# Optimization experiments

Hardware: AMD Instinct MI355X
Metric: run time of the kernel (lower is better)

## Reference

```python
import jax, jax.numpy as jnp
import numpy as np

MODEL_DIM = 1024
HEADS = 16
HEAD_DIM = MODEL_DIM // HEADS
SEQ = 1024


def setup_inputs() -> dict:
    key0 = jax.random.key(0)
    ks = jax.random.split(key0, 10)
    D, H, d, S = MODEL_DIM, HEADS, HEAD_DIM, SEQ
    s = 1.0 / np.sqrt(D)
    return {
        "value": jax.random.normal(ks[0], (S, D), dtype=jnp.float32),
        "key": jax.random.normal(ks[1], (S, D), dtype=jnp.float32),
        "query": jax.random.normal(ks[2], (S, D), dtype=jnp.float32),
        # per-head projection weights, torch Linear layout (out=d, in=D), stacked over heads
        "Wq": jax.random.uniform(ks[3], (H, d, D), jnp.float32, -s, s),
        "Wk": jax.random.uniform(ks[4], (H, d, D), jnp.float32, -s, s),
        "Wv": jax.random.uniform(ks[5], (H, d, D), jnp.float32, -s, s),
        # u, v biases: torch.rand -> uniform [0,1)
        "u": jax.random.uniform(ks[6], (H, d), dtype=jnp.float32),
        "v": jax.random.uniform(ks[7], (H, d), dtype=jnp.float32),
        "Wo": jax.random.uniform(ks[8], (D, D), jnp.float32, -s, s),
        "bo": jax.random.uniform(ks[9], (D,), jnp.float32, -s, s),
    }


def _rel_pos_R(d, Sq, Sk):
    # pos[i, j] = i - j (Transformer-XL style relative offsets)
    pos = (jnp.arange(Sq)[:, None] - jnp.arange(Sk)[None, :]).astype(jnp.float32)
    inv_freq = 10000.0 ** (-2.0 * jnp.arange(d // 2, dtype=jnp.float32) / d)  # (d/2,)
    ang = pos[None, :, :] * inv_freq[:, None, None]  # (d/2, Sq, Sk)
    # interleave: R[2i] = sin(ang_i), R[2i+1] = cos(ang_i)
    R = jnp.stack([jnp.sin(ang), jnp.cos(ang)], axis=1).reshape(d, Sq, Sk)
    return R


def reference(value, key, query, Wq, Wk, Wv, u, v, Wo, bo):
    # defaults of original forward: scale=True, mask=False
    H, d, D = Wq.shape
    Sq, Sk = query.shape[0], key.shape[0]
    q = jnp.einsum("hdD,sD->hsd", Wq, query)   # (H, Sq, d)
    k = jnp.einsum("hdD,tD->htd", Wk, key)     # (H, Sk, d)
    vals = jnp.einsum("hdD,tD->htd", Wv, value)  # (H, Sk, d)

    R = _rel_pos_R(d, Sq, Sk)  # (d, Sq, Sk)

    cc = jnp.einsum("hsd,htd->hst", q, k)       # content-content
    cp = jnp.einsum("hsd,dst->hst", q, R)       # content-position
    uk = jnp.einsum("hd,htd->ht", u, k)[:, None, :]  # global content bias
    vr = jnp.einsum("hd,dst->hst", v, R)        # global position bias

    att = (cc + cp + uk + vr) * (d ** -0.5)
    att = jax.nn.softmax(att, axis=2)

    out = jnp.einsum("hst,htd->hsd", att, vals)  # (H, Sq, d)
    out = out.transpose(1, 0, 2).reshape(Sq, H * d)  # concat heads along feature dim
    return out @ Wo.T + bo
```

## Files before the change

kernel.cpp:

```cpp
#include <hip/hip_runtime.h>
#include <math.h>

#define SQ 1024
#define DIM 1024
#define NH 16
#define HDIM 64

typedef short bf16x8 __attribute__((ext_vector_type(8)));
typedef float f32x4 __attribute__((ext_vector_type(4)));

__device__ __forceinline__ unsigned short f2bf(float x) {
  unsigned int u = __builtin_bit_cast(unsigned int, x);
  u += 0x7FFFu + ((u >> 16) & 1u);
  return (unsigned short)(u >> 16);
}
__device__ __forceinline__ unsigned int pkbf(float a, float b) {
  return (unsigned)f2bf(a) | ((unsigned)f2bf(b) << 16);
}

__global__ __launch_bounds__(256) void prep_kernel(
    const float* __restrict__ query, const float* __restrict__ key_,
    const float* __restrict__ value, const float* __restrict__ Wq,
    const float* __restrict__ Wk, const float* __restrict__ Wv,
    const float* __restrict__ Wo, unsigned short* __restrict__ bfin,
    unsigned short* __restrict__ Rc)
{
  const int b = blockIdx.x;
  if (b < 3584) {
    int gid = b * 256 + threadIdx.x;
    int seg = gid >> 17;
    int off = (gid & 131071) * 8;
    const float* s = seg == 0 ? query : seg == 1 ? key_ : seg == 2 ? value :
                     seg == 3 ? Wq : seg == 4 ? Wk : seg == 5 ? Wv : Wo;
    float4 a = *(const float4*)&s[off];
    float4 c = *(const float4*)&s[off + 4];
    uint4 o;
    o.x = pkbf(a.x, a.y); o.y = pkbf(a.z, a.w);
    o.z = pkbf(c.x, c.y); o.w = pkbf(c.z, c.w);
    *(uint4*)&bfin[(size_t)gid * 8] = o;
  } else {
    int gid = (b - 3584) * 256 + threadIdx.x;
    int p = gid >> 5, f = gid & 31;
    float pos = (float)(p - (SQ - 1));
    float invf = expf(-0.28782313662425575f * (float)f);
    float ang = pos * invf;
    Rc[p * HDIM + 2 * f]     = f2bf(sinf(ang));
    Rc[p * HDIM + 2 * f + 1] = f2bf(cosf(ang));
  }
}

__global__ __launch_bounds__(256) void gemm_qkv(
    const unsigned short* __restrict__ bfin,
    unsigned short* __restrict__ qu, unsigned short* __restrict__ qv,
    unsigned short* __restrict__ kkp, unsigned short* __restrict__ vvpT,
    const float* __restrict__ u, const float* __restrict__ v)
{
  __shared__ short As[64 * 72];
  __shared__ short Bs[64 * 72];
  const int z = blockIdx.z;
  const unsigned short* A = bfin + (size_t)z * (1 << 20);
  const unsigned short* B = bfin + (size_t)(3 + z) * (1 << 20);
  const int tid = threadIdx.x;
  const int bm = blockIdx.y * 64, bn = blockIdx.x * 64;
  const int w = tid >> 6, l = tid & 63, g = l >> 4, q = l & 15;
  const int wr = w >> 1, wc = w & 1;
  const int srow = tid >> 2, sc = (tid & 3) * 16;
  f32x4 acc[2][2] = {};

  for (int k0 = 0; k0 < DIM; k0 += 64) {
    __syncthreads();
    {
      const uint4* s0 = (const uint4*)&A[(bm + srow) * DIM + k0 + sc];
      *(uint4*)&As[srow * 72 + sc]     = s0[0];
      *(uint4*)&As[srow * 72 + sc + 8] = s0[1];
      const uint4* s1 = (const uint4*)&B[(bn + srow) * DIM + k0 + sc];
      *(uint4*)&Bs[srow * 72 + sc]     = s1[0];
      *(uint4*)&Bs[srow * 72 + sc + 8] = s1[1];
    }
    __syncthreads();
    #pragma unroll
    for (int ks = 0; ks < 2; ks++) {
      bf16x8 a0 = *(const bf16x8*)&As[(wr * 32 + q) * 72      + ks * 32 + g * 8];
      bf16x8 a1 = *(const bf16x8*)&As[(wr * 32 + 16 + q) * 72 + ks * 32 + g * 8];
      bf16x8 b0 = *(const bf16x8*)&Bs[(wc * 32 + q) * 72      + ks * 32 + g * 8];
      bf16x8 b1 = *(const bf16x8*)&Bs[(wc * 32 + 16 + q) * 72 + ks * 32 + g * 8];
      acc[0][0] = __builtin_amdgcn_mfma_f32_16x16x32_bf16(a0, b0, acc[0][0], 0, 0, 0);
      acc[0][1] = __builtin_amdgcn_mfma_f32_16x16x32_bf16(a0, b1, acc[0][1], 0, 0, 0);
      acc[1][0] = __builtin_amdgcn_mfma_f32_16x16x32_bf16(a1, b0, acc[1][0], 0, 0, 0);
      acc[1][1] = __builtin_amdgcn_mfma_f32_16x16x32_bf16(a1, b1, acc[1][1], 0, 0, 0);
    }
  }

  #pragma unroll
  for (int i = 0; i < 2; i++) {
    #pragma unroll
    for (int j = 0; j < 2; j++) {
      const int m0 = bm + wr * 32 + i * 16 + g * 4;
      const int n  = bn + wc * 32 + j * 16 + q;
      if (z == 0) {
        float uu = u[n], vv = v[n];
        #pragma unroll
        for (int r = 0; r < 4; r++) {
          qu[(m0 + r) * DIM + n] = f2bf((acc[i][j][r] + uu) * 0.125f);
          qv[(m0 + r) * DIM + n] = f2bf((acc[i][j][r] + vv) * 0.125f);
        }
      } else if (z == 1) {
        #pragma unroll
        for (int r = 0; r < 4; r++)
          kkp[(m0 + r) * DIM + n] = f2bf(acc[i][j][r]);
      } else {
        ushort4 pk;
        pk.x = f2bf(acc[i][j][0]); pk.y = f2bf(acc[i][j][1]);
        pk.z = f2bf(acc[i][j][2]); pk.w = f2bf(acc[i][j][3]);
        *(ushort4*)&vvpT[n * SQ + m0] = pk;
      }
    }
  }
}

__global__ __launch_bounds__(256) void gemm_out(
    const unsigned short* __restrict__ A, const unsigned short* __restrict__ B,
    float* __restrict__ out, const float* __restrict__ bo)
{
  __shared__ short As[64 * 72];
  __shared__ short Bs[64 * 72];
  const int tid = threadIdx.x;
  const int bm = blockIdx.y * 64, bn = blockIdx.x * 64;
  const int w = tid >> 6, l = tid & 63, g = l >> 4, q = l & 15;
  const int wr = w >> 1, wc = w & 1;
  const int srow = tid >> 2, sc = (tid & 3) * 16;
  f32x4 acc[2][2] = {};

  for (int k0 = 0; k0 < DIM; k0 += 64) {
    __syncthreads();
    {
      const uint4* s0 = (const uint4*)&A[(bm + srow) * DIM + k0 + sc];
      *(uint4*)&As[srow * 72 + sc]     = s0[0];
      *(uint4*)&As[srow * 72 + sc + 8] = s0[1];
      const uint4* s1 = (const uint4*)&B[(bn + srow) * DIM + k0 + sc];
      *(uint4*)&Bs[srow * 72 + sc]     = s1[0];
      *(uint4*)&Bs[srow * 72 + sc + 8] = s1[1];
    }
    __syncthreads();
    #pragma unroll
    for (int ks = 0; ks < 2; ks++) {
      bf16x8 a0 = *(const bf16x8*)&As[(wr * 32 + q) * 72      + ks * 32 + g * 8];
      bf16x8 a1 = *(const bf16x8*)&As[(wr * 32 + 16 + q) * 72 + ks * 32 + g * 8];
      bf16x8 b0 = *(const bf16x8*)&Bs[(wc * 32 + q) * 72      + ks * 32 + g * 8];
      bf16x8 b1 = *(const bf16x8*)&Bs[(wc * 32 + 16 + q) * 72 + ks * 32 + g * 8];
      acc[0][0] = __builtin_amdgcn_mfma_f32_16x16x32_bf16(a0, b0, acc[0][0], 0, 0, 0);
      acc[0][1] = __builtin_amdgcn_mfma_f32_16x16x32_bf16(a0, b1, acc[0][1], 0, 0, 0);
      acc[1][0] = __builtin_amdgcn_mfma_f32_16x16x32_bf16(a1, b0, acc[1][0], 0, 0, 0);
      acc[1][1] = __builtin_amdgcn_mfma_f32_16x16x32_bf16(a1, b1, acc[1][1], 0, 0, 0);
    }
  }

  #pragma unroll
  for (int i = 0; i < 2; i++) {
    #pragma unroll
    for (int j = 0; j < 2; j++) {
      const int m0 = bm + wr * 32 + i * 16 + g * 4;
      const int n  = bn + wc * 32 + j * 16 + q;
      float bb = bo[n];
      #pragma unroll
      for (int r = 0; r < 4; r++)
        out[(m0 + r) * DIM + n] = acc[i][j][r] + bb;
    }
  }
}

__global__ __launch_bounds__(256) void attn_mfma(
    const unsigned short* __restrict__ qu, const unsigned short* __restrict__ qv,
    const unsigned short* __restrict__ kkp, const unsigned short* __restrict__ vvpT,
    const unsigned short* __restrict__ Rc, unsigned short* __restrict__ attout)
{
  __shared__ short Ks[64 * 72];
  __shared__ short Vs[64 * 72];
  __shared__ short Rcs[128 * 72];
  __shared__ short Ps[64 * 72];
  __shared__ float Gs[64 * 84];

  const int tid = threadIdx.x;
  const int h  = blockIdx.x >> 4;
  const int s0 = (blockIdx.x & 15) * 64;
  const int w = tid >> 6, l = tid & 63, g = l >> 4, q = l & 15;
  const int col0 = h * HDIM;

  const int sw = s0 + w * 16 + q;
  bf16x8 qub[2], qvb[2];
  qub[0] = *(const bf16x8*)&qu[sw * DIM + col0 + g * 8];
  qub[1] = *(const bf16x8*)&qu[sw * DIM + col0 + 32 + g * 8];
  qvb[0] = *(const bf16x8*)&qv[sw * DIM + col0 + g * 8];
  qvb[1] = *(const bf16x8*)&qv[sw * DIM + col0 + 32 + g * 8];

  f32x4 accO[4] = {};
  float m_run = -1e30f, l_run = 0.f;

  const int srow = tid >> 2, sc = (tid & 3) * 16;
  const int rrow = tid >> 1, rc = (tid & 1) * 32;

  for (int t0 = 0; t0 < SQ; t0 += 64) {
    __syncthreads();
    {
      const uint4* ksrc = (const uint4*)&kkp[(t0 + srow) * DIM + col0 + sc];
      *(uint4*)&Ks[srow * 72 + sc]     = ksrc[0];
      *(uint4*)&Ks[srow * 72 + sc + 8] = ksrc[1];
      const uint4* vsrc = (const uint4*)&vvpT[(col0 + srow) * SQ + t0 + sc];
      *(uint4*)&Vs[srow * 72 + sc]     = vsrc[0];
      *(uint4*)&Vs[srow * 72 + sc + 8] = vsrc[1];
      const int P0 = s0 - t0 + 960;
      const uint4* rsrc = (const uint4*)&Rc[(P0 + rrow) * HDIM + rc];
      *(uint4*)&Rcs[rrow * 72 + rc]      = rsrc[0];
      *(uint4*)&Rcs[rrow * 72 + rc + 8]  = rsrc[1];
      *(uint4*)&Rcs[rrow * 72 + rc + 16] = rsrc[2];
      *(uint4*)&Rcs[rrow * 72 + rc + 24] = rsrc[3];
    }
    __syncthreads();

    f32x4 accS[4] = {};
    f32x4 accG[5] = {};
    #pragma unroll
    for (int ks = 0; ks < 2; ks++) {
      #pragma unroll
      for (int tf = 0; tf < 4; tf++) {
        bf16x8 a = *(const bf16x8*)&Ks[(tf * 16 + q) * 72 + ks * 32 + g * 8];
        accS[tf] = __builtin_amdgcn_mfma_f32_16x16x32_bf16(a, qub[ks], accS[tf], 0, 0, 0);
      }
      #pragma unroll
      for (int pf = 0; pf < 5; pf++) {
        bf16x8 a = *(const bf16x8*)&Rcs[(w * 16 + pf * 16 + q) * 72 + ks * 32 + g * 8];
        accG[pf] = __builtin_amdgcn_mfma_f32_16x16x32_bf16(a, qvb[ks], accG[pf], 0, 0, 0);
      }
    }
    #pragma unroll
    for (int pf = 0; pf < 5; pf++)
      *(f32x4*)&Gs[(w * 16 + q) * 84 + pf * 16 + g * 4] = accG[pf];

    float pvals[16];
    float mx = -1e30f;
    #pragma unroll
    for (int tf = 0; tf < 4; tf++) {
      #pragma unroll
      for (int r = 0; r < 4; r++) {
        int t_rel = tf * 16 + g * 4 + r;
        float sval = accS[tf][r] + Gs[(w * 16 + q) * 84 + (q - t_rel + 63)];
        pvals[tf * 4 + r] = sval;
        mx = fmaxf(mx, sval);
      }
    }
    mx = fmaxf(mx, __shfl_xor(mx, 16));
    mx = fmaxf(mx, __shfl_xor(mx, 32));
    float m_new = fmaxf(m_run, mx);
    float scale = __expf(m_run - m_new);
    float rsum = 0.f;
    #pragma unroll
    for (int i = 0; i < 16; i++) {
      float p = __expf(pvals[i] - m_new);
      pvals[i] = p;
      rsum += p;
    }
    rsum += __shfl_xor(rsum, 16);
    rsum += __shfl_xor(rsum, 32);
    l_run = l_run * scale + rsum;
    m_run = m_new;
    #pragma unroll
    for (int df = 0; df < 4; df++) {
      #pragma unroll
      for (int r = 0; r < 4; r++) accO[df][r] *= scale;
    }
    #pragma unroll
    for (int tf = 0; tf < 4; tf++) {
      unsigned int lo = pkbf(pvals[tf * 4 + 0], pvals[tf * 4 + 1]);
      unsigned int hi = pkbf(pvals[tf * 4 + 2], pvals[tf * 4 + 3]);
      *(uint2*)&Ps[(w * 16 + q) * 72 + tf * 16 + g * 4] = make_uint2(lo, hi);
    }
    #pragma unroll
    for (int ks = 0; ks < 2; ks++) {
      bf16x8 b = *(const bf16x8*)&Ps[(w * 16 + q) * 72 + ks * 32 + g * 8];
      #pragma unroll
      for (int df = 0; df < 4; df++) {
        bf16x8 a = *(const bf16x8*)&Vs[(df * 16 + q) * 72 + ks * 32 + g * 8];
        accO[df] = __builtin_amdgcn_mfma_f32_16x16x32_bf16(a, b, accO[df], 0, 0, 0);
      }
    }
  }

  const float inv = 1.f / l_run;
  #pragma unroll
  for (int df = 0; df < 4; df++) {
    unsigned int lo = pkbf(accO[df][0] * inv, accO[df][1] * inv);
    unsigned int hi = pkbf(accO[df][2] * inv, accO[df][3] * inv);
    *(uint2*)&attout[sw * DIM + col0 + df * 16 + g * 4] = make_uint2(lo, hi);
  }
}

extern "C" void kernel_launch(void* const* d_in, const int* in_sizes, int n_in,
                              void* d_out, int out_size, void* d_ws, size_t ws_size,
                              hipStream_t stream) {
  const float* value = (const float*)d_in[0];
  const float* key   = (const float*)d_in[1];
  const float* query = (const float*)d_in[2];
  const float* Wq    = (const float*)d_in[3];
  const float* Wk    = (const float*)d_in[4];
  const float* Wv    = (const float*)d_in[5];
  const float* u     = (const float*)d_in[6];
  const float* v     = (const float*)d_in[7];
  const float* Wo    = (const float*)d_in[8];
  const float* bo    = (const float*)d_in[9];
  float* out = (float*)d_out;

  unsigned short* ws = (unsigned short*)d_ws;
  unsigned short* bfin   = ws;
  unsigned short* qu_p   = bfin   + 7 * (1 << 20);
  unsigned short* qv_p   = qu_p   + (1 << 20);
  unsigned short* kkp    = qv_p   + (1 << 20);
  unsigned short* vvpT   = kkp    + (1 << 20);
  unsigned short* attout = vvpT   + (1 << 20);
  unsigned short* Rc     = attout + (1 << 20);

  prep_kernel<<<3840, 256, 0, stream>>>(query, key, value, Wq, Wk, Wv, Wo, bfin, Rc);

  dim3 gqkv(16, 16, 3);
  gemm_qkv<<<gqkv, 256, 0, stream>>>(bfin, qu_p, qv_p, kkp, vvpT, u, v);

  attn_mfma<<<NH * (SQ / 64), 256, 0, stream>>>(qu_p, qv_p, kkp, vvpT, Rc, attout);

  dim3 gg(16, 16);
  gemm_out<<<gg, 256, 0, stream>>>(attout, bfin + 6 * (1 << 20), out, bo);
}
```

Baseline: 164.1 us.

## Split attention key range across two blocks with flash-decoding style combine

The attention kernel previously launched 256 blocks, each sweeping all 1024 keys. It now splits the key range in two via blockIdx.y, writing unnormalized partial outputs plus running max and sum to fp32 workspace, and a new combine kernel merges the halves into bf16 output. This doubles the block count to fill more of the GPU's compute units and adds a launch-bounds occupancy hint, at the cost of extra global traffic for the partials and one more kernel launch.

```diff
diff --git a/kernel.cpp b/kernel.cpp
--- a/kernel.cpp
+++ b/kernel.cpp
@@ -169,10 +169,11 @@
   }
 }
 
-__global__ __launch_bounds__(256) void attn_mfma(
+__global__ __launch_bounds__(256, 2) void attn_mfma(
     const unsigned short* __restrict__ qu, const unsigned short* __restrict__ qv,
     const unsigned short* __restrict__ kkp, const unsigned short* __restrict__ vvpT,
-    const unsigned short* __restrict__ Rc, unsigned short* __restrict__ attout)
+    const unsigned short* __restrict__ Rc, float* __restrict__ PO,
+    float* __restrict__ ML)
 {
   __shared__ short Ks[64 * 72];
   __shared__ short Vs[64 * 72];
@@ -183,6 +184,7 @@
   const int tid = threadIdx.x;
   const int h  = blockIdx.x >> 4;
   const int s0 = (blockIdx.x & 15) * 64;
+  const int th = blockIdx.y;
   const int w = tid >> 6, l = tid & 63, g = l >> 4, q = l & 15;
   const int col0 = h * HDIM;
 
@@ -199,7 +201,7 @@
   const int srow = tid >> 2, sc = (tid & 3) * 16;
   const int rrow = tid >> 1, rc = (tid & 1) * 32;
 
-  for (int t0 = 0; t0 < SQ; t0 += 64) {
+  for (int t0 = th * 512; t0 < th * 512 + 512; t0 += 64) {
     __syncthreads();
     {
       const uint4* ksrc = (const uint4*)&kkp[(t0 + srow) * DIM + col0 + sc];
@@ -285,13 +287,41 @@
     }
   }
 
-  const float inv = 1.f / l_run;
+  const int tile = blockIdx.x * 2 + th;
+  float* POt = PO + (size_t)tile * 4096;
+  const int sl = w * 16 + q;
   #pragma unroll
-  for (int df = 0; df < 4; df++) {
-    unsigned int lo = pkbf(accO[df][0] * inv, accO[df][1] * inv);
-    unsigned int hi = pkbf(accO[df][2] * inv, accO[df][3] * inv);
-    *(uint2*)&attout[sw * DIM + col0 + df * 16 + g * 4] = make_uint2(lo, hi);
-  }
+  for (int df = 0; df < 4; df++)
+    *(f32x4*)&POt[sl * 64 + df * 16 + g * 4] = accO[df];
+  if (g == 0) {
+    ML[tile * 128 + sl * 2]     = m_run;
+    ML[tile * 128 + sl * 2 + 1] = l_run;
+  }
+}
+
+__global__ __launch_bounds__(256) void attn_combine(
+    const float* __restrict__ PO, const float* __restrict__ ML,
+    unsigned short* __restrict__ attout)
+{
+  int gid = blockIdx.x * 256 + threadIdx.x;
+  int s  = gid >> 8;
+  int c  = (gid & 255) * 4;
+  int h  = c >> 6;
+  int sb = s >> 6, sl = s & 63;
+  int tA = (h * 16 + sb) * 2, tB = tA + 1;
+  float mA = ML[tA * 128 + sl * 2], lA = ML[tA * 128 + sl * 2 + 1];
+  float mB = ML[tB * 128 + sl * 2], lB = ML[tB * 128 + sl * 2 + 1];
+  float m = fmaxf(mA, mB);
+  float wA = __expf(mA - m), wB = __expf(mB - m);
+  float inv = 1.f / (lA * wA + lB * wB);
+  wA *= inv; wB *= inv;
+  int dl = c & 63;
+  float4 a = *(const float4*)&PO[(size_t)tA * 4096 + sl * 64 + dl];
+  float4 b = *(const float4*)&PO[(size_t)tB * 4096 + sl * 64 + dl];
+  uint2 o;
+  o.x = pkbf(a.x * wA + b.x * wB, a.y * wA + b.y * wB);
+  o.y = pkbf(a.z * wA + b.z * wB, a.w * wA + b.w * wB);
+  *(uint2*)&attout[s * DIM + c] = o;
 }
 
 extern "C" void kernel_launch(void* const* d_in, const int* in_sizes, int n_in,
@@ -317,13 +347,17 @@
   unsigned short* vvpT   = kkp    + (1 << 20);
   unsigned short* attout = vvpT   + (1 << 20);
   unsigned short* Rc     = attout + (1 << 20);
+  float* PO = (float*)(Rc + 2048 * 64);
+  float* ML = PO + (size_t)512 * 4096;
 
   prep_kernel<<<3840, 256, 0, stream>>>(query, key, value, Wq, Wk, Wv, Wo, bfin, Rc);
 
   dim3 gqkv(16, 16, 3);
   gemm_qkv<<<gqkv, 256, 0, stream>>>(bfin, qu_p, qv_p, kkp, vvpT, u, v);
 
-  attn_mfma<<<NH * (SQ / 64), 256, 0, stream>>>(qu_p, qv_p, kkp, vvpT, Rc, attout);
+  dim3 gattn(NH * (SQ / 64), 2);
+  attn_mfma<<<gattn, 256, 0, stream>>>(qu_p, qv_p, kkp, vvpT, Rc, PO, ML);
+  attn_combine<<<1024, 256, 0, stream>>>(PO, ML, attout);
 
   dim3 gg(16, 16);
   gemm_out<<<gg, 256, 0, stream>>>(attout, bfin + 6 * (1 << 20), out, bo);
```

Result: faster. 158.0 us (-3.7%).
